# Kernel tuning notes

Measured on AMD Instinct MI355X. Metric: run time of the kernel, lower is better.

## Reference

```python
import jax, jax.numpy as jnp
import numpy as np

# model constants (par dict in original repo)
U = 0.45
U_STD = -0.55
ALPHA_STD = 0.006667   # dt / tau_std
ALPHA_STF = 0.05       # dt / tau_stf
DT = 10.0              # ms
TAU_MEM = 100.0        # ms

N_INPUT, N_HIDDEN, N_OUTPUT = 64, 256, 16
BATCH, T = 16, 64


def setup_inputs() -> dict:
    key = jax.random.key(0)
    ks = jax.random.split(key, 4)
    x = jax.random.normal(ks[0], (T, BATCH, N_INPUT), dtype=jnp.float32)
    # orthogonal-ish init is irrelevant for correctness; scaled gaussians suffice
    W_in = jax.random.normal(ks[1], (N_INPUT, N_HIDDEN), dtype=jnp.float32) / np.sqrt(N_INPUT)
    W_rec = jax.random.normal(ks[2], (N_HIDDEN, N_HIDDEN), dtype=jnp.float32) / np.sqrt(N_HIDDEN)
    W_bias = jnp.zeros((N_HIDDEN,), dtype=jnp.float32)
    W_out = jax.random.normal(ks[3], (N_HIDDEN, N_OUTPUT), dtype=jnp.float32) / np.sqrt(N_HIDDEN)
    W_out_b = jnp.zeros((N_OUTPUT,), dtype=jnp.float32)
    return {"x": x, "W_in": W_in, "W_rec": W_rec, "W_bias": W_bias,
            "W_out": W_out, "W_out_b": W_out_b}


def reference(x, W_in, W_rec, W_bias, W_out, W_out_b):
    B = x.shape[1]
    H = W_rec.shape[0]
    dt_s = DT / 1000.0
    dtm = DT / TAU_MEM

    h0 = jnp.zeros((B, H), x.dtype)
    sx0 = jnp.ones((B, H, H), x.dtype)                 # syn_x init
    su0 = jnp.full((B, H, H), U_STD + 1.0, x.dtype)    # syn_u init = U_std + 1

    def step(carry, inp):
        h, sx, su = carry
        # syn_x update: uses OLD syn_u, syn_x, h; h broadcast over last axis (presyn index i)
        sx_new = sx + ALPHA_STD * (1.0 - sx) - dt_s * (su * sx) * h[:, :, None]
        # syn_u update: batched matmul (U*(1-su)) @ Hmat where Hmat[b,i,j] = h[b,i]
        # -> result[b,i,j] = sum_k (U*(1-su))[b,i,k] * h[b,k], constant over j
        v = jnp.einsum('bik,bk->bi', U * (1.0 - su), h)
        su_new = su + ALPHA_STF * (U - su) + dt_s * v[:, :, None]
        sx_new = jnp.clip(sx_new, 0.0, 1.0)
        su_new = jnp.clip(su_new, 0.0, 1.0)
        # hidden update: h @ (syn_x*syn_u*W_rec) as (B,1,H)x(B,H,H)
        rec = jnp.einsum('bi,bij->bj', h, (sx_new * su_new) * W_rec)
        h_new = jax.nn.relu((1.0 - dtm) * h + dtm * (rec + W_bias) + inp @ W_in)
        y = jax.nn.sigmoid(h_new @ W_out + W_out_b)
        return (h_new, sx_new, su_new), (h_new, y, sx_new, su_new)

    _, (h_seq, y_seq, sx_seq, su_seq) = jax.lax.scan(step, (h0, sx0, su0), x)
    # prepend initial states to mirror the original lists (T+1 states, T outputs)
    h_all = jnp.concatenate([h0[None], h_seq], axis=0)
    sx_all = jnp.concatenate([sx0[None], sx_seq], axis=0)
    su_all = jnp.concatenate([su0[None], su_seq], axis=0)
    return h_all, y_seq, sx_all, su_all
```

## Files before the change

kernel.cpp:

```cpp
#include <hip/hip_runtime.h>

typedef _Float16 half2_t __attribute__((ext_vector_type(2)));
typedef float float4_t __attribute__((ext_vector_type(4)));
typedef unsigned long long u64;

#define U_PAR 0.45f
#define A_STD 0.006667f
#define A_STF 0.05f
#define DT_S  0.01f

#define T_STEPS 64
#define BATCH   16
#define NIN     64
#define NH      256
#define NOUT    16

#define H_OFF  0
#define H_SZ   ((T_STEPS + 1) * BATCH * NH)
#define Y_OFF  H_SZ
#define Y_SZ   (T_STEPS * BATCH * NOUT)
#define SX_OFF (Y_OFF + Y_SZ)
#define PLANE  ((T_STEPS + 1) * BATCH * NH)
#define SX_SZ  ((size_t)PLANE * NH)
#define SU_OFF ((size_t)SX_OFF + SX_SZ)

#define GROUP    32
#define N_ROWS   (2 * PLANE)
#define N_GROUPS (N_ROWS / GROUP)
#define TAG_BASE 0x5EED0000u

static __device__ __forceinline__ float fdot2f(half2_t a, half2_t b, float c) {
#if __has_builtin(__builtin_amdgcn_fdot2)
  return __builtin_amdgcn_fdot2(a, b, c, false);
#else
  return c + (float)a.x * (float)b.x + (float)a.y * (float)b.y;
#endif
}

static __device__ __forceinline__ void bar_lds() {
  asm volatile("s_waitcnt lgkmcnt(0)" ::: "memory");
  __builtin_amdgcn_s_barrier();
  asm volatile("" ::: "memory");
}

__global__ __launch_bounds__(256, 2) void rnn_fused(
    const float* __restrict__ x, const float* __restrict__ Win,
    const float* __restrict__ Wrec, const float* __restrict__ Wbias,
    const float* __restrict__ Wout, const float* __restrict__ Woutb,
    float* __restrict__ out, u64* __restrict__ wsx64, u64* __restrict__ wsu64)
{
  if (blockIdx.x < BATCH) {
    __builtin_amdgcn_s_setprio(1);
    const int b = blockIdx.x;
    const int j = threadIdx.x;
    const int wv = j >> 6, lane = j & 63;

    __shared__ __align__(16) _Float16 g_h[NH];
    __shared__ __align__(16) _Float16 x_h[NIN];
    __shared__ float hs[NH];
    __shared__ float red_s[4];
    __shared__ float ypart[4][NOUT];

    half2_t w2[128];
#pragma unroll
    for (int k = 0; k < 128; ++k) {
      float a0 = Wrec[(2 * k) * NH + j];
      float a1 = Wrec[(2 * k + 1) * NH + j];
      half2_t v; v.x = (_Float16)a0; v.y = (_Float16)a1;
      w2[k] = v;
    }
    half2_t win2[32];
#pragma unroll
    for (int k = 0; k < 32; ++k) {
      float a0 = Win[(2 * k) * NH + j];
      float a1 = Win[(2 * k + 1) * NH + j];
      half2_t v; v.x = (_Float16)a0; v.y = (_Float16)a1;
      win2[k] = v;
    }
    const int chunk = j >> 4, o = j & 15;
    float wseg[16];
#pragma unroll
    for (int m = 0; m < 16; ++m) wseg[m] = Wout[(chunk * 16 + m) * NOUT + o];
    const float bias = Wbias[j];

    float h = 0.f, sx = 1.f, su = U_PAR;
    out[H_OFF + b * NH + j] = 0.f;

    for (int t = 0; t < T_STEPS; ++t) {
      if (j < NIN) x_h[j] = (_Float16)x[(size_t)(t * BATCH + b) * NIN + j];
      float s = h;
#pragma unroll
      for (int m = 1; m < 64; m <<= 1) s += __shfl_xor(s, m, 64);
      if (lane == 0) red_s[wv] = s;
      bar_lds();

      float S = red_s[0] + red_s[1] + red_s[2] + red_s[3];
      float sxn = sx + A_STD * (1.f - sx) - DT_S * su * sx * h;
      float sun = su + A_STF * (U_PAR - su) + DT_S * (U_PAR * (1.f - su) * S);
      sxn = fminf(fmaxf(sxn, 0.f), 1.f);
      sun = fminf(fmaxf(sun, 0.f), 1.f);
      g_h[j] = (_Float16)(h * sxn * sun);
      const int row = (t + 1) * BATCH + b;
      {
        u64 tg = (u64)(TAG_BASE | (unsigned)row) << 32;
        u64 px = tg | (u64)__float_as_uint(sxn);
        u64 pu = tg | (u64)__float_as_uint(sun);
        __hip_atomic_store(&wsx64[(size_t)row * NH + j], px,
                           __ATOMIC_RELAXED, __HIP_MEMORY_SCOPE_AGENT);
        __hip_atomic_store(&wsu64[(size_t)row * NH + j], pu,
                           __ATOMIC_RELAXED, __HIP_MEMORY_SCOPE_AGENT);
      }
      sx = sxn; su = sun;

      float xw = 0.f;
      {
        const half2_t* x2 = (const half2_t*)x_h;
        float xa0 = 0.f, xa1 = 0.f;
#pragma unroll
        for (int k = 0; k < 32; k += 2) {
          xa0 = fdot2f(win2[k], x2[k], xa0);
          xa1 = fdot2f(win2[k + 1], x2[k + 1], xa1);
        }
        xw = xa0 + xa1;
      }
      bar_lds();

      float a0 = 0.f, a1 = 0.f, a2 = 0.f, a3 = 0.f;
      {
        const half2_t* g2 = (const half2_t*)g_h;
#pragma unroll
        for (int k = 0; k < 128; k += 4) {
          a0 = fdot2f(w2[k],     g2[k],     a0);
          a1 = fdot2f(w2[k + 1], g2[k + 1], a1);
          a2 = fdot2f(w2[k + 2], g2[k + 2], a2);
          a3 = fdot2f(w2[k + 3], g2[k + 3], a3);
        }
      }
      float rec = (a0 + a1) + (a2 + a3);
      float hn = fmaxf(0.9f * h + 0.1f * (rec + bias) + xw, 0.f);
      out[H_OFF + (size_t)row * NH + j] = hn;
      hs[j] = hn;
      h = hn;
      bar_lds();

      float yp = 0.f;
      {
        float y0 = 0.f, y1 = 0.f;
#pragma unroll
        for (int m = 0; m < 16; m += 2) {
          y0 = fmaf(hs[chunk * 16 + m],     wseg[m],     y0);
          y1 = fmaf(hs[chunk * 16 + m + 1], wseg[m + 1], y1);
        }
        yp = y0 + y1;
      }
      yp += __shfl_xor(yp, 16, 64);
      yp += __shfl_xor(yp, 32, 64);
      if (lane < NOUT) ypart[wv][lane] = yp;
      bar_lds();

      if (j < NOUT) {
        float v = ypart[0][j] + ypart[1][j] + ypart[2][j] + ypart[3][j] + Woutb[j];
        out[Y_OFF + (size_t)(t * BATCH + b) * NOUT + j] = 1.f / (1.f + expf(-v));
      }
    }
    __builtin_amdgcn_s_setprio(0);
  } else {
    const int nCons = (int)gridDim.x - BATCH;
    const int cb    = (int)blockIdx.x - BATCH;
    const int tid   = threadIdx.x;
    __shared__ float sval[2][GROUP];

    auto stageFn = [&](int g, int buf) {
      int r0    = g * GROUP;
      int t     = r0 >> 13;
      int rem   = r0 & 8191;
      int which = rem >> 12;
      int b     = (rem >> 8) & 15;
      int i0    = rem & 255;
      if (t == 0) {
        sval[buf][tid] = which ? U_PAR : 1.0f;
        return;
      }
      int row = (t << 4) | b;
      unsigned exp = TAG_BASE | (unsigned)row;
      const u64* src = (which ? wsu64 : wsx64) + (size_t)row * NH + i0 + tid;
      u64 v = __hip_atomic_load(src, __ATOMIC_RELAXED, __HIP_MEMORY_SCOPE_AGENT);
      while ((unsigned)(v >> 32) != exp) {
        __builtin_amdgcn_s_sleep(32);
        v = __hip_atomic_load(src, __ATOMIC_RELAXED, __HIP_MEMORY_SCOPE_AGENT);
      }
      sval[buf][tid] = __uint_as_float((unsigned)(v & 0xFFFFFFFFu));
    };

    if (cb < N_GROUPS && tid < GROUP) stageFn(cb, 0);
    int k = 0;
    for (int g = cb; g < N_GROUPS; g += nCons, ++k) {
      int buf = k & 1;
      bar_lds();
      int gn = g + nCons;
      if (gn < N_GROUPS && tid < GROUP) stageFn(gn, buf ^ 1);

      int r0    = g * GROUP;
      int t     = r0 >> 13;
      int rem   = r0 & 8191;
      int which = rem >> 12;
      int b     = (rem >> 8) & 15;
      int i0    = rem & 255;
      size_t rowbase = (size_t)(((t << 4) | b) * NH + i0);
      float* dstBase = out + (which ? SU_OFF : (size_t)SX_OFF) + rowbase * NH;
#pragma unroll
      for (int p = 0; p < 8; ++p) {
        int id = p * 256 + tid;
        int rr = id >> 6, c = id & 63;
        float v = sval[buf][rr];
        float4_t f4 = {v, v, v, v};
        __builtin_nontemporal_store(f4, (float4_t*)(dstBase + (size_t)rr * NH) + c);
      }
    }
  }
}

__global__ __launch_bounds__(512) void rnn_phase1(
    const float* __restrict__ x, const float* __restrict__ Win,
    const float* __restrict__ Wrec, const float* __restrict__ Wbias,
    float* __restrict__ out)
{
  const int b   = blockIdx.x;
  const int tid = threadIdx.x;
  const int j   = tid & 255;
  const int q   = tid >> 8;

  __shared__ __align__(16) _Float16 g_h[NH];
  __shared__ __align__(16) _Float16 x_h[NIN];
  __shared__ float p_s[NH];
  __shared__ float xw_s[NH];
  __shared__ float red_s[8];

  half2_t w2[64];
#pragma unroll
  for (int k = 0; k < 64; ++k) {
    float a0 = Wrec[(q * 128 + 2 * k) * NH + j];
    float a1 = Wrec[(q * 128 + 2 * k + 1) * NH + j];
    half2_t v; v.x = (_Float16)a0; v.y = (_Float16)a1;
    w2[k] = v;
  }
  half2_t win2[32];
  if (q == 1) {
#pragma unroll
    for (int k = 0; k < 32; ++k) {
      float a0 = Win[(2 * k) * NH + j];
      float a1 = Win[(2 * k + 1) * NH + j];
      half2_t v; v.x = (_Float16)a0; v.y = (_Float16)a1;
      win2[k] = v;
    }
  }

  float h = 0.f, sx = 1.f, su = U_PAR;
  float bias = 0.f;
  if (q == 0) bias = Wbias[j];

  if (q == 0) {
    out[H_OFF + b * NH + j] = 0.f;
    size_t row0 = (size_t)b * NH + j;
    out[SX_OFF + row0 * NH] = 1.f;
    out[SU_OFF + row0 * NH] = U_PAR;
  }

  for (int t = 0; t < T_STEPS; ++t) {
    if (q == 0) {
      float s = h;
#pragma unroll
      for (int m = 1; m < 64; m <<= 1) s += __shfl_xor(s, m, 64);
      if ((tid & 63) == 0) red_s[tid >> 6] = s;
    } else {
      if (j < NIN) x_h[j] = (_Float16)x[(size_t)(t * BATCH + b) * NIN + j];
    }
    __syncthreads();

    float partial = 0.f;
    if (q == 0) {
      float S   = red_s[0] + red_s[1] + red_s[2] + red_s[3];
      float sxn = sx + A_STD * (1.f - sx) - DT_S * su * sx * h;
      float v   = U_PAR * (1.f - su) * S;
      float sun = su + A_STF * (U_PAR - su) + DT_S * v;
      sxn = fminf(fmaxf(sxn, 0.f), 1.f);
      sun = fminf(fmaxf(sun, 0.f), 1.f);
      float g = h * sxn * sun;
      g_h[j] = (_Float16)g;
      sx = sxn; su = sun;
      size_t row = (size_t)((t + 1) * BATCH + b) * NH + j;
      out[SX_OFF + row * NH] = sxn;
      out[SU_OFF + row * NH] = sun;
    } else {
      float xw = 0.f;
      const half2_t* x2 = (const half2_t*)x_h;
#pragma unroll
      for (int k = 0; k < 32; ++k) xw = fdot2f(win2[k], x2[k], xw);
      xw_s[j] = xw;
    }
    __syncthreads();

    {
      const half2_t* g2 = (const half2_t*)g_h;
#pragma unroll
      for (int k = 0; k < 64; ++k) partial = fdot2f(w2[k], g2[q * 64 + k], partial);
    }
    if (q == 1) p_s[j] = partial;
    __syncthreads();

    if (q == 0) {
      float rec = partial + p_s[j];
      float hn  = 0.9f * h + 0.1f * (rec + bias) + xw_s[j];
      hn = fmaxf(hn, 0.f);
      out[H_OFF + ((size_t)(t + 1) * BATCH + b) * NH + j] = hn;
      h = hn;
    }
  }
}

__global__ __launch_bounds__(256) void rnn_yhead(
    const float* __restrict__ Wout, const float* __restrict__ Woutb,
    float* __restrict__ out)
{
  const int tb = blockIdx.x;
  const int t  = tb / BATCH, b = tb % BATCH;
  const int j  = threadIdx.x;
  __shared__ float red[NOUT][5];

  float h = out[H_OFF + ((size_t)(t + 1) * BATCH + b) * NH + j];
  const float* wrow = Wout + j * NOUT;
#pragma unroll
  for (int o = 0; o < NOUT; ++o) {
    float v = h * wrow[o];
#pragma unroll
    for (int m = 1; m < 64; m <<= 1) v += __shfl_xor(v, m, 64);
    if ((j & 63) == 0) red[o][j >> 6] = v;
  }
  __syncthreads();
  if (j < NOUT) {
    float v = red[j][0] + red[j][1] + red[j][2] + red[j][3] + Woutb[j];
    out[Y_OFF + (size_t)tb * NOUT + j] = 1.f / (1.f + expf(-v));
  }
}

__global__ __launch_bounds__(256) void rnn_bcast(float* __restrict__ out)
{
  const size_t base = SX_OFF;
  const int ROWS = 32;
  __shared__ float sval[ROWS];
  const int ngroups = (2 * PLANE) / ROWS;
  for (int grp = blockIdx.x; grp < ngroups; grp += gridDim.x) {
    size_t r0 = (size_t)grp * ROWS;
    if (threadIdx.x < ROWS) sval[threadIdx.x] = out[base + (r0 + threadIdx.x) * NH];
    __syncthreads();
#pragma unroll
    for (int p = 0; p < 8; ++p) {
      int id = p * 256 + threadIdx.x;
      int r = id >> 6, c = id & 63;
      float v = sval[r];
      float4_t f4 = {v, v, v, v};
      float4_t* dst = (float4_t*)(out + base + (r0 + r) * NH);
      __builtin_nontemporal_store(f4, dst + c);
    }
    __syncthreads();
  }
}

extern "C" void kernel_launch(void* const* d_in, const int* in_sizes, int n_in,
                              void* d_out, int out_size, void* d_ws, size_t ws_size,
                              hipStream_t stream) {
  (void)in_sizes; (void)n_in; (void)out_size;
  const float* x     = (const float*)d_in[0];
  const float* Win   = (const float*)d_in[1];
  const float* Wrec  = (const float*)d_in[2];
  const float* Wbias = (const float*)d_in[3];
  const float* Wout  = (const float*)d_in[4];
  const float* Woutb = (const float*)d_in[5];
  float* out = (float*)d_out;

  const size_t WS_NEED = 2 * (size_t)PLANE * sizeof(u64);
  u64* wsx64 = (u64*)d_ws;
  u64* wsu64 = wsx64 + PLANE;

  bool coop_ok = (ws_size >= WS_NEED);
  int dev = 0, cus = 0, occ = 0;
  if (coop_ok && hipGetDevice(&dev) != hipSuccess) coop_ok = false;
  if (coop_ok && hipDeviceGetAttribute(&cus, hipDeviceAttributeMultiprocessorCount,
                                       dev) != hipSuccess) coop_ok = false;
  if (coop_ok && hipOccupancyMaxActiveBlocksPerMultiprocessor(
                     &occ, (const void*)rnn_fused, 256, 0) != hipSuccess) coop_ok = false;
  int grid = occ * cus;
  if (grid > BATCH + 4096) grid = BATCH + 4096;
  if (grid < 80) coop_ok = false;

  if (coop_ok) {
    void* args[] = {(void*)&x, (void*)&Win, (void*)&Wrec, (void*)&Wbias,
                    (void*)&Wout, (void*)&Woutb, (void*)&out,
                    (void*)&wsx64, (void*)&wsu64};
    hipError_t e = hipLaunchCooperativeKernel((const void*)rnn_fused, dim3(grid),
                                              dim3(256), args, 0, stream);
    if (e == hipSuccess) return;
  }

  hipLaunchKernelGGL(rnn_phase1, dim3(BATCH), dim3(512), 0, stream,
                     x, Win, Wrec, Wbias, out);
  hipLaunchKernelGGL(rnn_yhead, dim3(T_STEPS * BATCH), dim3(256), 0, stream,
                     Wout, Woutb, out);
  hipLaunchKernelGGL(rnn_bcast, dim3(2048), dim3(256), 0, stream, out);
}
```

Measured before the change: 141.1 us.

## Hoist input projection and output head out of the serial recurrence loop

Before the time loop, the producer blocks now stage all of x and W_out in LDS and precompute the input projection for every timestep. The sigmoid output head runs in one batch after the recurrence, reading h values that were stored back into the same LDS buffer. This drops the per-step x load, the input dot products, the y reduction and two of the four barriers from the serial dependency chain. The larger LDS footprint (about 90KB) lowers occupancy, so the cooperative grid is now one block per CU, capped at 256. That leaves fewer consumer blocks for the large sx/su broadcast writes.

```diff
diff --git a/kernel.cpp b/kernel.cpp
--- a/kernel.cpp
+++ b/kernel.cpp
@@ -56,10 +56,10 @@
     const int wv = j >> 6, lane = j & 63;
 
     __shared__ __align__(16) _Float16 g_h[NH];
-    __shared__ __align__(16) _Float16 x_h[NIN];
-    __shared__ float hs[NH];
+    __shared__ __align__(16) _Float16 x16[T_STEPS * NIN];
+    __shared__ float xw_lds[T_STEPS * NH];
+    __shared__ float wout_s[NH * 17];
     __shared__ float red_s[4];
-    __shared__ float ypart[4][NOUT];
 
     half2_t w2[128];
 #pragma unroll
@@ -77,17 +77,35 @@
       half2_t v; v.x = (_Float16)a0; v.y = (_Float16)a1;
       win2[k] = v;
     }
-    const int chunk = j >> 4, o = j & 15;
-    float wseg[16];
-#pragma unroll
-    for (int m = 0; m < 16; ++m) wseg[m] = Wout[(chunk * 16 + m) * NOUT + o];
     const float bias = Wbias[j];
+
+#pragma unroll
+    for (int e = 0; e < 16; ++e) {
+      int idx = e * 256 + j;
+      int t = idx >> 6, i = idx & 63;
+      x16[idx] = (_Float16)x[(size_t)(t * BATCH + b) * NIN + i];
+    }
+#pragma unroll
+    for (int o = 0; o < NOUT; ++o) wout_s[j * 17 + o] = Wout[j * NOUT + o];
+    bar_lds();
+
+    {
+      const half2_t* xh2 = (const half2_t*)x16;
+      for (int t = 0; t < T_STEPS; ++t) {
+        float xa0 = 0.f, xa1 = 0.f;
+#pragma unroll
+        for (int k = 0; k < 32; k += 2) {
+          xa0 = fdot2f(win2[k],     xh2[t * 32 + k],     xa0);
+          xa1 = fdot2f(win2[k + 1], xh2[t * 32 + k + 1], xa1);
+        }
+        xw_lds[t * NH + j] = xa0 + xa1;
+      }
+    }
 
     float h = 0.f, sx = 1.f, su = U_PAR;
     out[H_OFF + b * NH + j] = 0.f;
 
     for (int t = 0; t < T_STEPS; ++t) {
-      if (j < NIN) x_h[j] = (_Float16)x[(size_t)(t * BATCH + b) * NIN + j];
       float s = h;
 #pragma unroll
       for (int m = 1; m < 64; m <<= 1) s += __shfl_xor(s, m, 64);
@@ -103,26 +121,15 @@
       const int row = (t + 1) * BATCH + b;
       {
         u64 tg = (u64)(TAG_BASE | (unsigned)row) << 32;
-        u64 px = tg | (u64)__float_as_uint(sxn);
-        u64 pu = tg | (u64)__float_as_uint(sun);
-        __hip_atomic_store(&wsx64[(size_t)row * NH + j], px,
+        __hip_atomic_store(&wsx64[(size_t)row * NH + j],
+                           tg | (u64)__float_as_uint(sxn),
                            __ATOMIC_RELAXED, __HIP_MEMORY_SCOPE_AGENT);
-        __hip_atomic_store(&wsu64[(size_t)row * NH + j], pu,
+        __hip_atomic_store(&wsu64[(size_t)row * NH + j],
+                           tg | (u64)__float_as_uint(sun),
                            __ATOMIC_RELAXED, __HIP_MEMORY_SCOPE_AGENT);
       }
       sx = sxn; su = sun;
-
-      float xw = 0.f;
-      {
-        const half2_t* x2 = (const half2_t*)x_h;
-        float xa0 = 0.f, xa1 = 0.f;
-#pragma unroll
-        for (int k = 0; k < 32; k += 2) {
-          xa0 = fdot2f(win2[k], x2[k], xa0);
-          xa1 = fdot2f(win2[k + 1], x2[k + 1], xa1);
-        }
-        xw = xa0 + xa1;
-      }
+      float xw = xw_lds[t * NH + j];
       bar_lds();
 
       float a0 = 0.f, a1 = 0.f, a2 = 0.f, a3 = 0.f;
@@ -139,28 +146,28 @@
       float rec = (a0 + a1) + (a2 + a3);
       float hn = fmaxf(0.9f * h + 0.1f * (rec + bias) + xw, 0.f);
       out[H_OFF + (size_t)row * NH + j] = hn;
-      hs[j] = hn;
+      xw_lds[t * NH + j] = hn;
       h = hn;
-      bar_lds();
-
-      float yp = 0.f;
-      {
-        float y0 = 0.f, y1 = 0.f;
-#pragma unroll
-        for (int m = 0; m < 16; m += 2) {
-          y0 = fmaf(hs[chunk * 16 + m],     wseg[m],     y0);
-          y1 = fmaf(hs[chunk * 16 + m + 1], wseg[m + 1], y1);
+    }
+
+    bar_lds();
+    {
+      const int o = lane & 15, part = lane >> 4;
+      const float wb = Woutb[o];
+      for (int tt = 0; tt < 16; ++tt) {
+        int t = wv * 16 + tt;
+        float acc = 0.f;
+#pragma unroll 8
+        for (int j2 = 0; j2 < 64; ++j2) {
+          int jj = part * 64 + j2;
+          acc = fmaf(xw_lds[t * NH + jj], wout_s[jj * 17 + o], acc);
         }
-        yp = y0 + y1;
-      }
-      yp += __shfl_xor(yp, 16, 64);
-      yp += __shfl_xor(yp, 32, 64);
-      if (lane < NOUT) ypart[wv][lane] = yp;
-      bar_lds();
-
-      if (j < NOUT) {
-        float v = ypart[0][j] + ypart[1][j] + ypart[2][j] + ypart[3][j] + Woutb[j];
-        out[Y_OFF + (size_t)(t * BATCH + b) * NOUT + j] = 1.f / (1.f + expf(-v));
+        acc += __shfl_xor(acc, 16, 64);
+        acc += __shfl_xor(acc, 32, 64);
+        if (lane < NOUT) {
+          out[Y_OFF + (size_t)(t * BATCH + b) * NOUT + lane] =
+              1.f / (1.f + expf(-(acc + wb)));
+        }
       }
     }
     __builtin_amdgcn_s_setprio(0);
@@ -389,8 +396,9 @@
                                        dev) != hipSuccess) coop_ok = false;
   if (coop_ok && hipOccupancyMaxActiveBlocksPerMultiprocessor(
                      &occ, (const void*)rnn_fused, 256, 0) != hipSuccess) coop_ok = false;
-  int grid = occ * cus;
-  if (grid > BATCH + 4096) grid = BATCH + 4096;
+  if (occ < 1) coop_ok = false;
+  int grid = cus;
+  if (grid > 256) grid = 256;
   if (grid < 80) coop_ok = false;
 
   if (coop_ok) {
```

Measured after the change: 179.2 us. 27.0% more time.
